# Kernel tuning notes

Hardware: AMD Instinct MI355X
Metric: run time of the kernel (lower is better)

The kernel has to match this reference:

```python
import jax, jax.numpy as jnp
import numpy as np

N = 50000
E = 1600000
IN_DIM = 256
HID = 64
OUT = 16
NEG_SLOPE = 0.01


def setup_inputs() -> dict:
    key = jax.random.key(0)
    ks = jax.random.split(key, 6)
    local_features = jax.random.normal(ks[0], (N, IN_DIM), dtype=jnp.float32)
    edge_index = jax.random.randint(ks[1], (2, E), 0, N, dtype=jnp.int32)
    W0 = jax.random.normal(ks[2], (IN_DIM, HID), dtype=jnp.float32) * 0.05
    a0 = jax.random.normal(ks[3], (2 * HID, 1), dtype=jnp.float32) * 0.05
    W1 = jax.random.normal(ks[4], (HID, OUT), dtype=jnp.float32) * 0.05
    a1 = jax.random.normal(ks[5], (2 * OUT, 1), dtype=jnp.float32) * 0.05
    return {"local_features": local_features, "edge_index": edge_index,
            "W0": W0, "a0": a0, "W1": W1, "a1": a1}


def _segment_softmax(scores, seg, num_segments):
    # softmax over edges sharing the same row (destination) id
    smax = jax.ops.segment_max(scores, seg, num_segments=num_segments)
    ex = jnp.exp(scores - smax[seg])
    ssum = jax.ops.segment_sum(ex, seg, num_segments=num_segments)
    return ex / ssum[seg]


def _gat_layer(H, row, col, W, a, apply_elu):
    d = W.shape[1]
    Hw = H @ W                                   # [N, d]
    # score_e = leaky_relu([Hw[row] || Hw[col]] @ a) = leaky_relu(pr[row] + pc[col])
    pr = Hw @ a[:d, 0]                           # [N]
    pc = Hw @ a[d:, 0]                           # [N]
    s = pr[row] + pc[col]                        # [E]
    s = jnp.where(s >= 0, s, NEG_SLOPE * s)      # leaky_relu
    att = _segment_softmax(s, row, Hw.shape[0])  # per-row sparse softmax (dim=1)
    # out[row] = sum_e att_e * Hw[col_e]
    out = jax.ops.segment_sum(att[:, None] * Hw[col], row, num_segments=Hw.shape[0])
    if apply_elu:
        out = jnp.where(out > 0, out, jnp.expm1(out))  # elu
    return out


def reference(local_features, edge_index, W0, a0, W1, a1):
    row = edge_index[0]
    col = edge_index[1]
    H = _gat_layer(local_features, row, col, W0, a0, apply_elu=True)
    H = _gat_layer(H, row, col, W1, a1, apply_elu=False)
    return jax.nn.log_softmax(H, axis=1)
```

## Files before the change

kernel.cpp:

```cpp
#include <hip/hip_runtime.h>
#include <hip/hip_bf16.h>
#include <math.h>

#define NN 50000
#define NE 1600000
#define BSH 9
#define BCK 98
#define BCAP 20480

typedef __attribute__((ext_vector_type(8))) short bf16x8;
typedef __attribute__((ext_vector_type(4))) float f32x4;

__device__ __forceinline__ short f2bf(float f) {
    return (short)((__float_as_uint(f) + 0x8000u) >> 16);
}
__device__ __forceinline__ float bf2f(ushort u) {
    return __uint_as_float(((unsigned)u) << 16);
}
__device__ __forceinline__ unsigned enc_f(float f) {
    unsigned u = __float_as_uint(f);
    return (u & 0x80000000u) ? ~u : (u | 0x80000000u);
}
__device__ __forceinline__ float dec_f(unsigned e) {
    return (e & 0x80000000u) ? __uint_as_float(e & 0x7FFFFFFFu)
                             : __uint_as_float(~e);
}

__global__ void initcur_kernel(int* __restrict__ gcursor) {
    int b = threadIdx.x;
    if (b < BCK) gcursor[b] = b * BCAP;
}

__global__ void __launch_bounds__(1024) binA_kernel(
        const int* __restrict__ row, const int* __restrict__ col,
        int* __restrict__ gcursor, unsigned* __restrict__ staging) {
    __shared__ unsigned lds_stage[8192];
    __shared__ unsigned lds_addr[8192];
    __shared__ int lds_cnt[128];
    __shared__ int lds_off[128];
    __shared__ int wg_goff[128];
    __shared__ int wtot[2];
    int t = threadIdx.x;
    int lane = t & 63;
    int w = t >> 6;

    for (int cb = blockIdx.x * 8192; cb < NE; cb += gridDim.x * 8192) {
        int cnt_edges = NE - cb; if (cnt_edges > 8192) cnt_edges = 8192;
        if (t < 128) lds_cnt[t] = 0;
        __syncthreads();
        int myb[8]; int mylo[8]; unsigned mypk[8];
        #pragma unroll
        for (int i = 0; i < 8; ++i) {
            int idx = i * 1024 + t;
            myb[i] = -1;
            if (idx < cnt_edges) {
                int e = cb + idx;
                int r = row[e], c = col[e];
                int b = r >> BSH;
                myb[i] = b;
                mypk[i] = ((unsigned)(r & 511) << 16) | (unsigned)c;
                mylo[i] = atomicAdd(&lds_cnt[b], 1);
            }
        }
        __syncthreads();
        int v = (t < 128) ? lds_cnt[t] : 0;
        int x = v;
        #pragma unroll
        for (int off = 1; off < 64; off <<= 1) {
            int y = __shfl_up(x, off);
            if (lane >= off) x += y;
        }
        if (t < 128 && lane == 63) wtot[w] = x;
        __syncthreads();
        int add = (w == 1) ? wtot[0] : 0;
        if (t < 128) lds_off[t] = x - v + add;
        if (t < BCK) {
            int cc = lds_cnt[t];
            wg_goff[t] = cc ? atomicAdd(&gcursor[t], cc) : 0;
        }
        __syncthreads();
        #pragma unroll
        for (int i = 0; i < 8; ++i) if (myb[i] >= 0) {
            int p = lds_off[myb[i]] + mylo[i];
            lds_stage[p] = mypk[i];
            lds_addr[p] = (unsigned)(wg_goff[myb[i]] + mylo[i]);
        }
        __syncthreads();
        for (int i = t; i < cnt_edges; i += 1024)
            staging[lds_addr[i]] = lds_stage[i];
        __syncthreads();
    }
}

__global__ void bucketscan_kernel(const int* __restrict__ gcursor,
                                  int* __restrict__ bbase,
                                  int* __restrict__ rowptr) {
    __shared__ int wt0;
    int t = threadIdx.x;
    int lane = t & 63;
    int w = t >> 6;
    int v = (t < BCK) ? (gcursor[t] - t * BCAP) : 0;
    int x = v;
    #pragma unroll
    for (int off = 1; off < 64; off <<= 1) {
        int y = __shfl_up(x, off);
        if (lane >= off) x += y;
    }
    if (w == 0 && lane == 63) wt0 = x;
    __syncthreads();
    int excl = x - v + ((w == 1) ? wt0 : 0);
    if (t < BCK) bbase[t] = excl;
    if (t == BCK - 1) { bbase[BCK] = excl + v; rowptr[NN] = excl + v; }
}

__global__ void __launch_bounds__(1024) binB_kernel(
        const int* __restrict__ bbase,
        const unsigned* __restrict__ staging,
        int* __restrict__ rowptr,
        ushort* __restrict__ colperm) {
    __shared__ int cur[512];
    __shared__ int lexcl[512];
    __shared__ int wls[8];
    __shared__ ushort lds_col[BCAP];
    int b = blockIdx.x;
    int t = threadIdx.x;
    int lane = t & 63;
    int w = t >> 6;
    int rbase = b << BSH;
    int nrows = NN - rbase; if (nrows > 512) nrows = 512;
    int gbase = bbase[b];
    int cnt = bbase[b + 1] - gbase;
    if (cnt > BCAP) cnt = BCAP;
    const unsigned* sb = staging + (size_t)b * BCAP;

    if (t < 512) cur[t] = 0;
    __syncthreads();
    for (int i = t; i < cnt; i += 1024)
        atomicAdd(&cur[sb[i] >> 16], 1);
    __syncthreads();
    int v = 0, x = 0;
    if (t < 512) {
        v = cur[t];
        x = v;
        #pragma unroll
        for (int off = 1; off < 64; off <<= 1) {
            int y = __shfl_up(x, off);
            if (lane >= off) x += y;
        }
        if (lane == 63) wls[w] = x;
    }
    __syncthreads();
    if (t < 8) {
        int s = wls[t];
        #pragma unroll
        for (int off = 1; off < 8; off <<= 1) {
            int y = __shfl_up(s, off, 8);
            if ((t & 7) >= off) s += y;
        }
        wls[t] = s;
    }
    __syncthreads();
    if (t < 512) {
        int e = x - v + ((w > 0) ? wls[w - 1] : 0);
        lexcl[t] = e;
        if (t < nrows) rowptr[rbase + t] = gbase + e;
    }
    __syncthreads();
    if (t < 512) cur[t] = lexcl[t];
    __syncthreads();
    for (int i = t; i < cnt; i += 1024) {
        unsigned e = sb[i];
        int pos = atomicAdd(&cur[e >> 16], 1);
        lds_col[pos] = (ushort)(e & 0xFFFFu);
    }
    __syncthreads();
    for (int i = t; i < cnt; i += 1024)
        colperm[gbase + i] = lds_col[i];
}

__global__ void pcmax_kernel(const float* __restrict__ pc, unsigned* __restrict__ out) {
    int i = blockIdx.x * 256 + threadIdx.x;
    float v = (i < NN) ? pc[i] : -1e30f;
    #pragma unroll
    for (int off = 32; off; off >>= 1) v = fmaxf(v, __shfl_xor(v, off));
    if ((threadIdx.x & 63) == 0) atomicMax(out, enc_f(v));
}

__global__ void __launch_bounds__(256) gemm0_kernel(
        const float* __restrict__ X,
        const float* __restrict__ W,
        const float* __restrict__ a,
        __hip_bfloat16* __restrict__ Hwb,
        float* __restrict__ pr,
        float* __restrict__ pc) {
    __shared__ ushort Wt[64 * 264];
    int tid = threadIdx.x;
    int lane = tid & 63;
    int wid = tid >> 6;
    int c = lane & 15;
    int quad = lane >> 4;

    for (int i = tid; i < 256 * 64; i += 256) {
        int k = i >> 6, n = i & 63;
        Wt[n * 264 + k] = (ushort)f2bf(W[i]);
    }
    __syncthreads();

    int row0 = blockIdx.x * 64 + wid * 16;
    int arow = row0 + c; if (arow >= NN) arow = NN - 1;
    const float* xbase = X + (size_t)arow * 256 + quad * 8;
    const ushort* wt0 = &Wt[(0 * 16 + c) * 264 + quad * 8];
    const ushort* wt1 = &Wt[(1 * 16 + c) * 264 + quad * 8];
    const ushort* wt2 = &Wt[(2 * 16 + c) * 264 + quad * 8];
    const ushort* wt3 = &Wt[(3 * 16 + c) * 264 + quad * 8];

    f32x4 acc0 = {0.f,0.f,0.f,0.f}, acc1 = {0.f,0.f,0.f,0.f};
    f32x4 acc2 = {0.f,0.f,0.f,0.f}, acc3 = {0.f,0.f,0.f,0.f};

#pragma unroll
    for (int k0 = 0; k0 < 256; k0 += 32) {
        float4 xa = *(const float4*)(xbase + k0);
        float4 xb = *(const float4*)(xbase + k0 + 4);
        bf16x8 af;
        af[0] = f2bf(xa.x); af[1] = f2bf(xa.y); af[2] = f2bf(xa.z); af[3] = f2bf(xa.w);
        af[4] = f2bf(xb.x); af[5] = f2bf(xb.y); af[6] = f2bf(xb.z); af[7] = f2bf(xb.w);
        bf16x8 b0 = *(const bf16x8*)(wt0 + k0);
        bf16x8 b1 = *(const bf16x8*)(wt1 + k0);
        bf16x8 b2 = *(const bf16x8*)(wt2 + k0);
        bf16x8 b3 = *(const bf16x8*)(wt3 + k0);
        acc0 = __builtin_amdgcn_mfma_f32_16x16x32_bf16(af, b0, acc0, 0, 0, 0);
        acc1 = __builtin_amdgcn_mfma_f32_16x16x32_bf16(af, b1, acc1, 0, 0, 0);
        acc2 = __builtin_amdgcn_mfma_f32_16x16x32_bf16(af, b2, acc2, 0, 0, 0);
        acc3 = __builtin_amdgcn_mfma_f32_16x16x32_bf16(af, b3, acc3, 0, 0, 0);
    }

    float aA0 = a[c],      aA1 = a[16 + c],      aA2 = a[32 + c],      aA3 = a[48 + c];
    float aB0 = a[64 + c], aB1 = a[80 + c],      aB2 = a[96 + c],      aB3 = a[112 + c];

#pragma unroll
    for (int r = 0; r < 4; ++r) {
        int row = row0 + quad * 4 + r;
        float v0 = acc0[r], v1 = acc1[r], v2 = acc2[r], v3 = acc3[r];
        if (row < NN) {
            __hip_bfloat16* hp = Hwb + (size_t)row * 64 + c;
            hp[0]  = __float2bfloat16(v0);
            hp[16] = __float2bfloat16(v1);
            hp[32] = __float2bfloat16(v2);
            hp[48] = __float2bfloat16(v3);
        }
        float pv = v0 * aA0 + v1 * aA1 + v2 * aA2 + v3 * aA3;
        float qv = v0 * aB0 + v1 * aB1 + v2 * aB2 + v3 * aB3;
#pragma unroll
        for (int off = 8; off; off >>= 1) {
            pv += __shfl_xor(pv, off);
            qv += __shfl_xor(qv, off);
        }
        if (c == 0 && row < NN) { pr[row] = pv; pc[row] = qv; }
    }
}

__global__ void __launch_bounds__(256) node0_kernel(
        const int* __restrict__ rowptr,
        const ushort* __restrict__ colperm,
        const float* __restrict__ pr,
        const float* __restrict__ pc,
        const unsigned* __restrict__ pcmax,
        const ushort* __restrict__ Hwb,
        const float* __restrict__ W1,
        const float* __restrict__ a1,
        __hip_bfloat16* __restrict__ Hw1b,
        float* __restrict__ pr1,
        float* __restrict__ pc1) {
    __shared__ float W1s[64 * 17];
    __shared__ float a1s[32];
    __shared__ float hbuf[4][64];
    __shared__ unsigned long long wcbuf[4][64];
    int t = threadIdx.x;
    for (int i = t; i < 64 * 16; i += 256)
        W1s[(i >> 4) * 17 + (i & 15)] = W1[i];
    if (t < 32) a1s[t] = a1[t];
    __syncthreads();

    int lane = t & 63;
    int wid = t >> 6;
    int node = blockIdx.x * 4 + wid;
    if (node >= NN) return;
    int k = lane & 15, q = lane >> 4;
    int start = rowptr[node], end = rowptr[node + 1];
    float pri = pr[node];
    float m = pri + dec_f(*pcmax);
    m = (m >= 0.f) ? m : 0.01f * m;

    float wsum = 0.f;
    float acc0 = 0.f, acc1 = 0.f, acc2 = 0.f, acc3 = 0.f;
    for (int base = start; base < end; base += 64) {
        int n = end - base; if (n > 64) n = 64;
        float wv = 0.f; unsigned cv = 0;
        if (lane < n) {
            cv = (unsigned)colperm[base + lane];
            float s = pri + pc[cv];
            s = (s >= 0.f) ? s : 0.01f * s;
            wv = expf(s - m);
        }
        wsum += wv;
        wcbuf[wid][lane] = ((unsigned long long)cv << 32) |
                           (unsigned long long)__float_as_uint(wv);
        int iters = (n + 3) >> 2;
        #pragma unroll 4
        for (int jj = 0; jj < iters; ++jj) {
            unsigned long long wc = wcbuf[wid][jj * 4 + q];
            float wj = __uint_as_float((unsigned)wc);
            int cj = (int)(wc >> 32);
            ushort4 hv = *(const ushort4*)(Hwb + (size_t)cj * 64 + k * 4);
            acc0 = fmaf(wj, bf2f(hv.x), acc0);
            acc1 = fmaf(wj, bf2f(hv.y), acc1);
            acc2 = fmaf(wj, bf2f(hv.z), acc2);
            acc3 = fmaf(wj, bf2f(hv.w), acc3);
        }
    }
#pragma unroll
    for (int off = 32; off; off >>= 1) wsum += __shfl_xor(wsum, off);
    acc0 += __shfl_xor(acc0, 16); acc0 += __shfl_xor(acc0, 32);
    acc1 += __shfl_xor(acc1, 16); acc1 += __shfl_xor(acc1, 32);
    acc2 += __shfl_xor(acc2, 16); acc2 += __shfl_xor(acc2, 32);
    acc3 += __shfl_xor(acc3, 16); acc3 += __shfl_xor(acc3, 32);

    float inv = (wsum > 0.f) ? 1.f / wsum : 0.f;
    float h0 = acc0 * inv; h0 = (h0 > 0.f) ? h0 : expm1f(h0);
    float h1 = acc1 * inv; h1 = (h1 > 0.f) ? h1 : expm1f(h1);
    float h2 = acc2 * inv; h2 = (h2 > 0.f) ? h2 : expm1f(h2);
    float h3 = acc3 * inv; h3 = (h3 > 0.f) ? h3 : expm1f(h3);
    if (q == 0) {
        float4 hh = {h0, h1, h2, h3};
        *(float4*)&hbuf[wid][k * 4] = hh;
    }
    float vj = 0.f;
    const float* hb = hbuf[wid];
#pragma unroll
    for (int i = 0; i < 16; ++i) {
        int kk = q * 16 + i;
        vj = fmaf(hb[kk], W1s[kk * 17 + k], vj);
    }
    vj += __shfl_xor(vj, 16);
    vj += __shfl_xor(vj, 32);
    if (q == 0) Hw1b[(size_t)node * 16 + k] = __float2bfloat16(vj);
    float pv = vj * a1s[k];
    float qv = vj * a1s[16 + k];
#pragma unroll
    for (int off = 8; off; off >>= 1) {
        pv += __shfl_xor(pv, off);
        qv += __shfl_xor(qv, off);
    }
    if (lane == 0) { pr1[node] = pv; pc1[node] = qv; }
}

__global__ void __launch_bounds__(256) node1_kernel(
        const int* __restrict__ rowptr,
        const ushort* __restrict__ colperm,
        const float* __restrict__ pr,
        const float* __restrict__ pc,
        const unsigned* __restrict__ pcmax,
        const ushort* __restrict__ Hwb,
        float* __restrict__ out) {
    __shared__ unsigned long long wcbuf[4][64];
    int lane = threadIdx.x & 63;
    int wid = threadIdx.x >> 6;
    int node = blockIdx.x * 4 + wid;
    if (node >= NN) return;
    int k = lane & 15, q = lane >> 4;
    int start = rowptr[node], end = rowptr[node + 1];
    float pri = pr[node];
    float m = pri + dec_f(*pcmax);
    m = (m >= 0.f) ? m : 0.01f * m;

    float wsum = 0.f, acc = 0.f;
    for (int base = start; base < end; base += 64) {
        int n = end - base; if (n > 64) n = 64;
        float wv = 0.f; unsigned cv = 0;
        if (lane < n) {
            cv = (unsigned)colperm[base + lane];
            float s = pri + pc[cv];
            s = (s >= 0.f) ? s : 0.01f * s;
            wv = expf(s - m);
        }
        wsum += wv;
        wcbuf[wid][lane] = ((unsigned long long)cv << 32) |
                           (unsigned long long)__float_as_uint(wv);
        int iters = (n + 3) >> 2;
        #pragma unroll 4
        for (int jj = 0; jj < iters; ++jj) {
            unsigned long long wc = wcbuf[wid][jj * 4 + q];
            float wj = __uint_as_float((unsigned)wc);
            int cj = (int)(wc >> 32);
            float hj = bf2f(Hwb[(size_t)cj * 16 + k]);
            acc = fmaf(wj, hj, acc);
        }
    }
#pragma unroll
    for (int off = 32; off; off >>= 1) wsum += __shfl_xor(wsum, off);
    acc += __shfl_xor(acc, 16);
    acc += __shfl_xor(acc, 32);
    float v = (wsum > 0.f) ? acc / wsum : 0.f;
    float mm = v;
#pragma unroll
    for (int off = 8; off; off >>= 1) mm = fmaxf(mm, __shfl_xor(mm, off, 16));
    float ex = expf(v - mm);
    float ssx = ex;
#pragma unroll
    for (int off = 8; off; off >>= 1) ssx += __shfl_xor(ssx, off, 16);
    float r = v - (mm + logf(ssx));
    if (lane < 16) out[(size_t)node * 16 + k] = r;
}

extern "C" void kernel_launch(void* const* d_in, const int* in_sizes, int n_in,
                              void* d_out, int out_size, void* d_ws, size_t ws_size,
                              hipStream_t stream) {
    const float* X  = (const float*)d_in[0];
    const int*   ei = (const int*)d_in[1];
    const float* W0 = (const float*)d_in[2];
    const float* a0 = (const float*)d_in[3];
    const float* W1 = (const float*)d_in[4];
    const float* a1 = (const float*)d_in[5];
    float* out = (float*)d_out;

    const int* row = ei;
    const int* col = ei + NE;

    char* wsb = (char*)d_ws;
    size_t off = 0;
    auto alloc = [&](size_t bytes) {
        void* p = wsb + off;
        off += (bytes + 15) & ~(size_t)15;
        return p;
    };
    unsigned* maxes = (unsigned*)alloc(16);
    int* rowptr     = (int*)alloc((NN + 2) * 4);
    int* gcursor    = (int*)alloc(128 * 4);
    int* bbase      = (int*)alloc(128 * 4);
    unsigned* staging = (unsigned*)alloc((size_t)BCK * BCAP * 4);
    ushort* colperm = (ushort*)alloc((size_t)NE * 2);
    __hip_bfloat16* Hw0b = (__hip_bfloat16*)alloc((size_t)NN * 64 * 2);
    float* pr0      = (float*)alloc(NN * 4);
    float* pc0      = (float*)alloc(NN * 4);
    __hip_bfloat16* Hw1b = (__hip_bfloat16*)alloc((size_t)NN * 16 * 2);
    float* pr1      = (float*)alloc(NN * 4);
    float* pc1      = (float*)alloc(NN * 4);

    hipMemsetAsync(maxes, 0, 16, stream);

    initcur_kernel<<<1, 128, 0, stream>>>(gcursor);
    binA_kernel<<<196, 1024, 0, stream>>>(row, col, gcursor, staging);
    bucketscan_kernel<<<1, 128, 0, stream>>>(gcursor, bbase, rowptr);
    binB_kernel<<<BCK, 1024, 0, stream>>>(bbase, staging, rowptr, colperm);

    gemm0_kernel<<<(NN + 63) / 64, 256, 0, stream>>>(X, W0, a0, Hw0b, pr0, pc0);
    pcmax_kernel<<<(NN + 255) / 256, 256, 0, stream>>>(pc0, &maxes[0]);
    node0_kernel<<<(NN + 3) / 4, 256, 0, stream>>>(rowptr, colperm, pr0, pc0,
                                                   &maxes[0], (const ushort*)Hw0b,
                                                   W1, a1, Hw1b, pr1, pc1);

    pcmax_kernel<<<(NN + 255) / 256, 256, 0, stream>>>(pc1, &maxes[1]);
    node1_kernel<<<(NN + 3) / 4, 256, 0, stream>>>(rowptr, colperm, pr1, pc1,
                                                   &maxes[1], (const ushort*)Hw1b, out);
}
```

Baseline: 229.6 us.

## Fuse pc max reductions into producers, pre-transpose W0, widen gather loads

The two pcmax kernels are removed. The max of pc is now computed inside gemm0 and node0 with a block-level reduction followed by one atomic per block. A small prep kernel converts and transposes W0 to bf16 once, so each gemm0 block copies it into LDS directly, and each gemm0 block now covers 128 rows, which amortises that load. The gather loops in node0 and node1 read 8 or 2 bf16 values per lane with wider loads over 8 lanes per edge, and the memset is folded into initcur. The bounds checks on node are dropped because NN is divisible by 4.

```diff
diff --git a/kernel.cpp b/kernel.cpp
--- a/kernel.cpp
+++ b/kernel.cpp
@@ -14,9 +14,8 @@
 __device__ __forceinline__ short f2bf(float f) {
     return (short)((__float_as_uint(f) + 0x8000u) >> 16);
 }
-__device__ __forceinline__ float bf2f(ushort u) {
-    return __uint_as_float(((unsigned)u) << 16);
-}
+__device__ __forceinline__ float lo16(unsigned u) { return __uint_as_float(u << 16); }
+__device__ __forceinline__ float hi16(unsigned u) { return __uint_as_float(u & 0xffff0000u); }
 __device__ __forceinline__ unsigned enc_f(float f) {
     unsigned u = __float_as_uint(f);
     return (u & 0x80000000u) ? ~u : (u | 0x80000000u);
@@ -26,9 +25,10 @@
                              : __uint_as_float(~e);
 }
 
-__global__ void initcur_kernel(int* __restrict__ gcursor) {
+__global__ void initcur_kernel(int* __restrict__ gcursor, unsigned* __restrict__ maxes) {
     int b = threadIdx.x;
     if (b < BCK) gcursor[b] = b * BCAP;
+    if (b < 2) maxes[b] = 0u;
 }
 
 __global__ void __launch_bounds__(1024) binA_kernel(
@@ -178,85 +178,93 @@
         colperm[gbase + i] = lds_col[i];
 }
 
-__global__ void pcmax_kernel(const float* __restrict__ pc, unsigned* __restrict__ out) {
+__global__ void prep_kernel(const float* __restrict__ W, ushort* __restrict__ WTg) {
     int i = blockIdx.x * 256 + threadIdx.x;
-    float v = (i < NN) ? pc[i] : -1e30f;
-    #pragma unroll
-    for (int off = 32; off; off >>= 1) v = fmaxf(v, __shfl_xor(v, off));
-    if ((threadIdx.x & 63) == 0) atomicMax(out, enc_f(v));
+    if (i >= 64 * 256) return;
+    int n = i >> 8, k = i & 255;
+    WTg[n * 264 + k] = (ushort)f2bf(W[k * 64 + n]);
 }
 
 __global__ void __launch_bounds__(256) gemm0_kernel(
         const float* __restrict__ X,
-        const float* __restrict__ W,
+        const ushort* __restrict__ WTg,
         const float* __restrict__ a,
         __hip_bfloat16* __restrict__ Hwb,
         float* __restrict__ pr,
-        float* __restrict__ pc) {
+        float* __restrict__ pc,
+        unsigned* __restrict__ max0) {
     __shared__ ushort Wt[64 * 264];
+    __shared__ unsigned bmax;
     int tid = threadIdx.x;
-    int lane = tid & 63;
-    int wid = tid >> 6;
-    int c = lane & 15;
-    int quad = lane >> 4;
-
-    for (int i = tid; i < 256 * 64; i += 256) {
-        int k = i >> 6, n = i & 63;
-        Wt[n * 264 + k] = (ushort)f2bf(W[i]);
-    }
-    __syncthreads();
-
-    int row0 = blockIdx.x * 64 + wid * 16;
-    int arow = row0 + c; if (arow >= NN) arow = NN - 1;
-    const float* xbase = X + (size_t)arow * 256 + quad * 8;
-    const ushort* wt0 = &Wt[(0 * 16 + c) * 264 + quad * 8];
-    const ushort* wt1 = &Wt[(1 * 16 + c) * 264 + quad * 8];
-    const ushort* wt2 = &Wt[(2 * 16 + c) * 264 + quad * 8];
-    const ushort* wt3 = &Wt[(3 * 16 + c) * 264 + quad * 8];
-
-    f32x4 acc0 = {0.f,0.f,0.f,0.f}, acc1 = {0.f,0.f,0.f,0.f};
-    f32x4 acc2 = {0.f,0.f,0.f,0.f}, acc3 = {0.f,0.f,0.f,0.f};
-
-#pragma unroll
-    for (int k0 = 0; k0 < 256; k0 += 32) {
-        float4 xa = *(const float4*)(xbase + k0);
-        float4 xb = *(const float4*)(xbase + k0 + 4);
-        bf16x8 af;
-        af[0] = f2bf(xa.x); af[1] = f2bf(xa.y); af[2] = f2bf(xa.z); af[3] = f2bf(xa.w);
-        af[4] = f2bf(xb.x); af[5] = f2bf(xb.y); af[6] = f2bf(xb.z); af[7] = f2bf(xb.w);
-        bf16x8 b0 = *(const bf16x8*)(wt0 + k0);
-        bf16x8 b1 = *(const bf16x8*)(wt1 + k0);
-        bf16x8 b2 = *(const bf16x8*)(wt2 + k0);
-        bf16x8 b3 = *(const bf16x8*)(wt3 + k0);
-        acc0 = __builtin_amdgcn_mfma_f32_16x16x32_bf16(af, b0, acc0, 0, 0, 0);
-        acc1 = __builtin_amdgcn_mfma_f32_16x16x32_bf16(af, b1, acc1, 0, 0, 0);
-        acc2 = __builtin_amdgcn_mfma_f32_16x16x32_bf16(af, b2, acc2, 0, 0, 0);
-        acc3 = __builtin_amdgcn_mfma_f32_16x16x32_bf16(af, b3, acc3, 0, 0, 0);
-    }
-
-    float aA0 = a[c],      aA1 = a[16 + c],      aA2 = a[32 + c],      aA3 = a[48 + c];
-    float aB0 = a[64 + c], aB1 = a[80 + c],      aB2 = a[96 + c],      aB3 = a[112 + c];
-
-#pragma unroll
-    for (int r = 0; r < 4; ++r) {
-        int row = row0 + quad * 4 + r;
-        float v0 = acc0[r], v1 = acc1[r], v2 = acc2[r], v3 = acc3[r];
-        if (row < NN) {
-            __hip_bfloat16* hp = Hwb + (size_t)row * 64 + c;
-            hp[0]  = __float2bfloat16(v0);
-            hp[16] = __float2bfloat16(v1);
-            hp[32] = __float2bfloat16(v2);
-            hp[48] = __float2bfloat16(v3);
-        }
-        float pv = v0 * aA0 + v1 * aA1 + v2 * aA2 + v3 * aA3;
-        float qv = v0 * aB0 + v1 * aB1 + v2 * aB2 + v3 * aB3;
-#pragma unroll
-        for (int off = 8; off; off >>= 1) {
-            pv += __shfl_xor(pv, off);
-            qv += __shfl_xor(qv, off);
-        }
-        if (c == 0 && row < NN) { pr[row] = pv; pc[row] = qv; }
-    }
+    if (tid == 0) bmax = 0u;
+    {
+        const uint* src = (const uint*)WTg;
+        uint* dst = (uint*)Wt;
+        for (int i = tid; i < 64 * 132; i += 256) dst[i] = src[i];
+    }
+    __syncthreads();
+    int lane = tid & 63, wid = tid >> 6;
+    int c = lane & 15, quad = lane >> 4;
+    const ushort* wtp[4];
+#pragma unroll
+    for (int g = 0; g < 4; ++g) wtp[g] = &Wt[(g * 16 + c) * 264 + quad * 8];
+    float aA[4], aB[4];
+#pragma unroll
+    for (int g = 0; g < 4; ++g) { aA[g] = a[g * 16 + c]; aB[g] = a[64 + g * 16 + c]; }
+
+    int row0 = blockIdx.x * 128 + wid * 16;
+    float qmax = -1e30f;
+
+#pragma unroll
+    for (int tt = 0; tt < 2; ++tt) {
+        int rt = row0 + tt * 64;
+        int arow = rt + c; if (arow >= NN) arow = NN - 1;
+        const float* xbase = X + (size_t)arow * 256 + quad * 8;
+        f32x4 acc[4];
+#pragma unroll
+        for (int g = 0; g < 4; ++g) acc[g] = (f32x4){0.f, 0.f, 0.f, 0.f};
+
+#pragma unroll
+        for (int k0 = 0; k0 < 256; k0 += 32) {
+            float4 xa = *(const float4*)(xbase + k0);
+            float4 xb = *(const float4*)(xbase + k0 + 4);
+            bf16x8 af;
+            af[0] = f2bf(xa.x); af[1] = f2bf(xa.y); af[2] = f2bf(xa.z); af[3] = f2bf(xa.w);
+            af[4] = f2bf(xb.x); af[5] = f2bf(xb.y); af[6] = f2bf(xb.z); af[7] = f2bf(xb.w);
+#pragma unroll
+            for (int g = 0; g < 4; ++g) {
+                bf16x8 bg = *(const bf16x8*)(wtp[g] + k0);
+                acc[g] = __builtin_amdgcn_mfma_f32_16x16x32_bf16(af, bg, acc[g], 0, 0, 0);
+            }
+        }
+
+#pragma unroll
+        for (int r = 0; r < 4; ++r) {
+            int row = rt + quad * 4 + r;
+            float v0 = acc[0][r], v1 = acc[1][r], v2 = acc[2][r], v3 = acc[3][r];
+            if (row < NN) {
+                __hip_bfloat16* hp = Hwb + (size_t)row * 64 + c;
+                hp[0]  = __float2bfloat16(v0);
+                hp[16] = __float2bfloat16(v1);
+                hp[32] = __float2bfloat16(v2);
+                hp[48] = __float2bfloat16(v3);
+            }
+            float pv = v0 * aA[0] + v1 * aA[1] + v2 * aA[2] + v3 * aA[3];
+            float qv = v0 * aB[0] + v1 * aB[1] + v2 * aB[2] + v3 * aB[3];
+#pragma unroll
+            for (int off = 8; off; off >>= 1) {
+                pv += __shfl_xor(pv, off);
+                qv += __shfl_xor(qv, off);
+            }
+            if (c == 0 && row < NN) { pr[row] = pv; pc[row] = qv; }
+            qmax = fmaxf(qmax, qv);
+        }
+    }
+    qmax = fmaxf(qmax, __shfl_xor(qmax, 16));
+    qmax = fmaxf(qmax, __shfl_xor(qmax, 32));
+    if (lane == 0) atomicMax(&bmax, enc_f(qmax));
+    __syncthreads();
+    if (tid == 0) atomicMax(max0, bmax);
 }
 
 __global__ void __launch_bounds__(256) node0_kernel(
@@ -270,12 +278,15 @@
         const float* __restrict__ a1,
         __hip_bfloat16* __restrict__ Hw1b,
         float* __restrict__ pr1,
-        float* __restrict__ pc1) {
+        float* __restrict__ pc1,
+        unsigned* __restrict__ max1) {
     __shared__ float W1s[64 * 17];
     __shared__ float a1s[32];
     __shared__ float hbuf[4][64];
     __shared__ unsigned long long wcbuf[4][64];
+    __shared__ unsigned bmax;
     int t = threadIdx.x;
+    if (t == 0) bmax = 0u;
     for (int i = t; i < 64 * 16; i += 256)
         W1s[(i >> 4) * 17 + (i & 15)] = W1[i];
     if (t < 32) a1s[t] = a1[t];
@@ -284,15 +295,17 @@
     int lane = t & 63;
     int wid = t >> 6;
     int node = blockIdx.x * 4 + wid;
-    if (node >= NN) return;
-    int k = lane & 15, q = lane >> 4;
+    int k = lane & 7, q = lane >> 3;
     int start = rowptr[node], end = rowptr[node + 1];
     float pri = pr[node];
     float m = pri + dec_f(*pcmax);
     m = (m >= 0.f) ? m : 0.01f * m;
 
     float wsum = 0.f;
-    float acc0 = 0.f, acc1 = 0.f, acc2 = 0.f, acc3 = 0.f;
+    float acc[8];
+#pragma unroll
+    for (int i = 0; i < 8; ++i) acc[i] = 0.f;
+
     for (int base = start; base < end; base += 64) {
         int n = end - base; if (n > 64) n = 64;
         float wv = 0.f; unsigned cv = 0;
@@ -305,53 +318,65 @@
         wsum += wv;
         wcbuf[wid][lane] = ((unsigned long long)cv << 32) |
                            (unsigned long long)__float_as_uint(wv);
-        int iters = (n + 3) >> 2;
-        #pragma unroll 4
+        int iters = (n + 7) >> 3;
+        #pragma unroll 8
         for (int jj = 0; jj < iters; ++jj) {
-            unsigned long long wc = wcbuf[wid][jj * 4 + q];
+            unsigned long long wc = wcbuf[wid][jj * 8 + q];
             float wj = __uint_as_float((unsigned)wc);
             int cj = (int)(wc >> 32);
-            ushort4 hv = *(const ushort4*)(Hwb + (size_t)cj * 64 + k * 4);
-            acc0 = fmaf(wj, bf2f(hv.x), acc0);
-            acc1 = fmaf(wj, bf2f(hv.y), acc1);
-            acc2 = fmaf(wj, bf2f(hv.z), acc2);
-            acc3 = fmaf(wj, bf2f(hv.w), acc3);
+            uint4 hv = *(const uint4*)(Hwb + (size_t)cj * 64 + k * 8);
+            acc[0] = fmaf(wj, lo16(hv.x), acc[0]);
+            acc[1] = fmaf(wj, hi16(hv.x), acc[1]);
+            acc[2] = fmaf(wj, lo16(hv.y), acc[2]);
+            acc[3] = fmaf(wj, hi16(hv.y), acc[3]);
+            acc[4] = fmaf(wj, lo16(hv.z), acc[4]);
+            acc[5] = fmaf(wj, hi16(hv.z), acc[5]);
+            acc[6] = fmaf(wj, lo16(hv.w), acc[6]);
+            acc[7] = fmaf(wj, hi16(hv.w), acc[7]);
         }
     }
 #pragma unroll
     for (int off = 32; off; off >>= 1) wsum += __shfl_xor(wsum, off);
-    acc0 += __shfl_xor(acc0, 16); acc0 += __shfl_xor(acc0, 32);
-    acc1 += __shfl_xor(acc1, 16); acc1 += __shfl_xor(acc1, 32);
-    acc2 += __shfl_xor(acc2, 16); acc2 += __shfl_xor(acc2, 32);
-    acc3 += __shfl_xor(acc3, 16); acc3 += __shfl_xor(acc3, 32);
-
+#pragma unroll
+    for (int i = 0; i < 8; ++i) {
+        acc[i] += __shfl_xor(acc[i], 8);
+        acc[i] += __shfl_xor(acc[i], 16);
+        acc[i] += __shfl_xor(acc[i], 32);
+    }
     float inv = (wsum > 0.f) ? 1.f / wsum : 0.f;
-    float h0 = acc0 * inv; h0 = (h0 > 0.f) ? h0 : expm1f(h0);
-    float h1 = acc1 * inv; h1 = (h1 > 0.f) ? h1 : expm1f(h1);
-    float h2 = acc2 * inv; h2 = (h2 > 0.f) ? h2 : expm1f(h2);
-    float h3 = acc3 * inv; h3 = (h3 > 0.f) ? h3 : expm1f(h3);
-    if (q == 0) {
-        float4 hh = {h0, h1, h2, h3};
-        *(float4*)&hbuf[wid][k * 4] = hh;
-    }
+    float h[8];
+#pragma unroll
+    for (int i = 0; i < 8; ++i) {
+        float x = acc[i] * inv;
+        h[i] = (x > 0.f) ? x : expm1f(x);
+    }
+    if (lane < 8) {
+        float4 ha = {h[0], h[1], h[2], h[3]};
+        float4 hb = {h[4], h[5], h[6], h[7]};
+        *(float4*)&hbuf[wid][lane * 8] = ha;
+        *(float4*)&hbuf[wid][lane * 8 + 4] = hb;
+    }
+    int j = lane & 15, p = lane >> 4;
+    const float* hbp = hbuf[wid];
     float vj = 0.f;
-    const float* hb = hbuf[wid];
 #pragma unroll
     for (int i = 0; i < 16; ++i) {
-        int kk = q * 16 + i;
-        vj = fmaf(hb[kk], W1s[kk * 17 + k], vj);
+        int kk = p * 16 + i;
+        vj = fmaf(hbp[kk], W1s[kk * 17 + j], vj);
     }
     vj += __shfl_xor(vj, 16);
     vj += __shfl_xor(vj, 32);
-    if (q == 0) Hw1b[(size_t)node * 16 + k] = __float2bfloat16(vj);
-    float pv = vj * a1s[k];
-    float qv = vj * a1s[16 + k];
+    if (p == 0) Hw1b[(size_t)node * 16 + j] = __float2bfloat16(vj);
+    float pv = vj * a1s[j];
+    float qv = vj * a1s[16 + j];
 #pragma unroll
     for (int off = 8; off; off >>= 1) {
         pv += __shfl_xor(pv, off);
         qv += __shfl_xor(qv, off);
     }
-    if (lane == 0) { pr1[node] = pv; pc1[node] = qv; }
+    if (lane == 0) { pr1[node] = pv; pc1[node] = qv; atomicMax(&bmax, enc_f(qv)); }
+    __syncthreads();
+    if (t == 0) atomicMax(max1, bmax);
 }
 
 __global__ void __launch_bounds__(256) node1_kernel(
@@ -366,14 +391,13 @@
     int lane = threadIdx.x & 63;
     int wid = threadIdx.x >> 6;
     int node = blockIdx.x * 4 + wid;
-    if (node >= NN) return;
-    int k = lane & 15, q = lane >> 4;
+    int k = lane & 7, q = lane >> 3;
     int start = rowptr[node], end = rowptr[node + 1];
     float pri = pr[node];
     float m = pri + dec_f(*pcmax);
     m = (m >= 0.f) ? m : 0.01f * m;
 
-    float wsum = 0.f, acc = 0.f;
+    float wsum = 0.f, a0 = 0.f, a1 = 0.f;
     for (int base = start; base < end; base += 64) {
         int n = end - base; if (n > 64) n = 64;
         float wv = 0.f; unsigned cv = 0;
@@ -386,30 +410,34 @@
         wsum += wv;
         wcbuf[wid][lane] = ((unsigned long long)cv << 32) |
                            (unsigned long long)__float_as_uint(wv);
-        int iters = (n + 3) >> 2;
-        #pragma unroll 4
+        int iters = (n + 7) >> 3;
+        #pragma unroll 8
         for (int jj = 0; jj < iters; ++jj) {
-            unsigned long long wc = wcbuf[wid][jj * 4 + q];
+            unsigned long long wc = wcbuf[wid][jj * 8 + q];
             float wj = __uint_as_float((unsigned)wc);
             int cj = (int)(wc >> 32);
-            float hj = bf2f(Hwb[(size_t)cj * 16 + k]);
-            acc = fmaf(wj, hj, acc);
+            unsigned hv = *(const unsigned*)(Hwb + (size_t)cj * 16 + k * 2);
+            a0 = fmaf(wj, lo16(hv), a0);
+            a1 = fmaf(wj, hi16(hv), a1);
         }
     }
 #pragma unroll
     for (int off = 32; off; off >>= 1) wsum += __shfl_xor(wsum, off);
-    acc += __shfl_xor(acc, 16);
-    acc += __shfl_xor(acc, 32);
-    float v = (wsum > 0.f) ? acc / wsum : 0.f;
-    float mm = v;
-#pragma unroll
-    for (int off = 8; off; off >>= 1) mm = fmaxf(mm, __shfl_xor(mm, off, 16));
-    float ex = expf(v - mm);
-    float ssx = ex;
-#pragma unroll
-    for (int off = 8; off; off >>= 1) ssx += __shfl_xor(ssx, off, 16);
-    float r = v - (mm + logf(ssx));
-    if (lane < 16) out[(size_t)node * 16 + k] = r;
+    a0 += __shfl_xor(a0, 8); a0 += __shfl_xor(a0, 16); a0 += __shfl_xor(a0, 32);
+    a1 += __shfl_xor(a1, 8); a1 += __shfl_xor(a1, 16); a1 += __shfl_xor(a1, 32);
+    float inv = (wsum > 0.f) ? 1.f / wsum : 0.f;
+    float v0 = a0 * inv, v1 = a1 * inv;
+    float mm = fmaxf(v0, v1);
+#pragma unroll
+    for (int off = 1; off < 8; off <<= 1) mm = fmaxf(mm, __shfl_xor(mm, off, 8));
+    float ssx = expf(v0 - mm) + expf(v1 - mm);
+#pragma unroll
+    for (int off = 1; off < 8; off <<= 1) ssx += __shfl_xor(ssx, off, 8);
+    float lse = mm + logf(ssx);
+    if (q == 0) {
+        float2 o = {v0 - lse, v1 - lse};
+        *(float2*)(out + (size_t)node * 16 + k * 2) = o;
+    }
 }
 
 extern "C" void kernel_launch(void* const* d_in, const int* in_sizes, int n_in,
@@ -439,6 +467,7 @@
     int* bbase      = (int*)alloc(128 * 4);
     unsigned* staging = (unsigned*)alloc((size_t)BCK * BCAP * 4);
     ushort* colperm = (ushort*)alloc((size_t)NE * 2);
+    ushort* WTg     = (ushort*)alloc((size_t)64 * 264 * 2);
     __hip_bfloat16* Hw0b = (__hip_bfloat16*)alloc((size_t)NN * 64 * 2);
     float* pr0      = (float*)alloc(NN * 4);
     float* pc0      = (float*)alloc(NN * 4);
@@ -446,20 +475,18 @@
     float* pr1      = (float*)alloc(NN * 4);
     float* pc1      = (float*)alloc(NN * 4);
 
-    hipMemsetAsync(maxes, 0, 16, stream);
-
-    initcur_kernel<<<1, 128, 0, stream>>>(gcursor);
+    initcur_kernel<<<1, 128, 0, stream>>>(gcursor, maxes);
     binA_kernel<<<196, 1024, 0, stream>>>(row, col, gcursor, staging);
     bucketscan_kernel<<<1, 128, 0, stream>>>(gcursor, bbase, rowptr);
     binB_kernel<<<BCK, 1024, 0, stream>>>(bbase, staging, rowptr, colperm);
 
-    gemm0_kernel<<<(NN + 63) / 64, 256, 0, stream>>>(X, W0, a0, Hw0b, pr0, pc0);
-    pcmax_kernel<<<(NN + 255) / 256, 256, 0, stream>>>(pc0, &maxes[0]);
-    node0_kernel<<<(NN + 3) / 4, 256, 0, stream>>>(rowptr, colperm, pr0, pc0,
-                                                   &maxes[0], (const ushort*)Hw0b,
-                                                   W1, a1, Hw1b, pr1, pc1);
-
-    pcmax_kernel<<<(NN + 255) / 256, 256, 0, stream>>>(pc1, &maxes[1]);
-    node1_kernel<<<(NN + 3) / 4, 256, 0, stream>>>(rowptr, colperm, pr1, pc1,
-                                                   &maxes[1], (const ushort*)Hw1b, out);
-}
+    prep_kernel<<<64, 256, 0, stream>>>(W0, WTg);
+    gemm0_kernel<<<(NN + 127) / 128, 256, 0, stream>>>(X, WTg, a0, Hw0b, pr0, pc0,
+                                                       &maxes[0]);
+    node0_kernel<<<NN / 4, 256, 0, stream>>>(rowptr, colperm, pr0, pc0,
+                                             &maxes[0], (const ushort*)Hw0b,
+                                             W1, a1, Hw1b, pr1, pc1, &maxes[1]);
+
+    node1_kernel<<<NN / 4, 256, 0, stream>>>(rowptr, colperm, pr1, pc1,
+                                             &maxes[1], (const ushort*)Hw1b, out);
+}
```

Result: slower. 323.9 us (+41.1%).
